# Kernel tuning notes

Hardware: AMD Instinct MI355X
Metric: run time of the kernel (lower is better)

The kernel has to match this reference:

```python
import jax, jax.numpy as jnp
import numpy as np

B, T, E, H, D = 2, 2048, 1024, 16, 64  # D = attention_dim // num_heads

def setup_inputs() -> dict:
    key = jax.random.key(0)
    k1, k2, k3, k4 = jax.random.split(key, 4)
    scale = 1.0 / np.sqrt(E)  # ~ torch Linear init scale
    embedded = jax.random.normal(k1, (B, T, E), dtype=jnp.float32)
    Wq = jax.random.normal(k2, (H, D, E), dtype=jnp.float32) * scale
    Wk = jax.random.normal(k3, (H, D, E), dtype=jnp.float32) * scale
    Wv = jax.random.normal(k4, (H, D, E), dtype=jnp.float32) * scale
    return {"embedded": embedded, "Wq": Wq, "Wk": Wk, "Wv": Wv}

def reference(embedded, Wq, Wk, Wv):
    # Batched multi-head projection (original loops per head; same math).
    q = jnp.einsum('bte,hde->bhtd', embedded, Wq)
    k = jnp.einsum('bte,hde->bhtd', embedded, Wk)
    v = jnp.einsum('bte,hde->bhtd', embedded, Wv)
    scores = jnp.einsum('bhtd,bhsd->bhts', q, k) / jnp.sqrt(jnp.float32(D))
    causal = jnp.tril(jnp.ones((T, T), dtype=bool))  # [T,T]
    scores = jnp.where(causal, scores, -jnp.inf)
    attn = jax.nn.softmax(scores, axis=-1)
    out = jnp.einsum('bhts,bhsd->bhtd', attn, v)
    # concat heads on last dim: [B,T,H*D]
    return out.transpose(0, 2, 1, 3).reshape(B, T, H * D)
```

## Files before the change

kernel.cpp:

```cpp
#include <hip/hip_runtime.h>
#include <hip/hip_bf16.h>
#include <stdint.h>

typedef __bf16 bf16_t;
typedef __bf16 bf16x8 __attribute__((ext_vector_type(8)));
typedef float  f32x4  __attribute__((ext_vector_type(4)));

#define LOG2E 1.44269504088896f

__device__ __forceinline__ void gload_lds16(const void* g, void* l) {
    __builtin_amdgcn_global_load_lds(
        (__attribute__((address_space(1))) unsigned int*)(uintptr_t)g,
        (__attribute__((address_space(3))) unsigned int*)(uint32_t)(uintptr_t)l,
        16, 0, 0);
}

__global__ __launch_bounds__(256) void convert_kernel(
    const float* __restrict__ emb, const float* __restrict__ wq,
    const float* __restrict__ wk,  const float* __restrict__ wv,
    bf16_t* __restrict__ embb, bf16_t* __restrict__ wcat)
{
    size_t base = ((size_t)blockIdx.x * 256 + threadIdx.x) * 8;
    const float* src;
    bf16_t* dst;
    if (base < (size_t)4194304) { src = emb + base; dst = embb + base; }
    else {
        size_t r = base - 4194304;
        int wsel = (int)(r >> 20);
        size_t off = r & 1048575;
        src = (wsel == 0 ? wq : (wsel == 1 ? wk : wv)) + off;
        dst = wcat + r;
    }
    float4 a  = *(const float4*)src;
    float4 c2 = *(const float4*)(src + 4);
    bf16x8 o;
    o[0]=(bf16_t)a.x;  o[1]=(bf16_t)a.y;  o[2]=(bf16_t)a.z;  o[3]=(bf16_t)a.w;
    o[4]=(bf16_t)c2.x; o[5]=(bf16_t)c2.y; o[6]=(bf16_t)c2.z; o[7]=(bf16_t)c2.w;
    *(bf16x8*)dst = o;
}

__global__ __launch_bounds__(256, 3) void proj_kernel(
    const bf16_t* __restrict__ A, const bf16_t* __restrict__ Wc,
    bf16_t* __restrict__ qo, bf16_t* __restrict__ ko, bf16_t* __restrict__ vto)
{
    __shared__ __align__(128) char smem[32768];

    const int tid  = threadIdx.x;
    const int w    = tid >> 6, lane = tid & 63;
    const int wr   = w >> 1,  wc2  = w & 1;
    const int g    = lane >> 4, c = lane & 15;
    const int bm   = blockIdx.x & 31, bn = blockIdx.x >> 5;
    const int m0   = bm * 128, n0 = bn * 128;

    f32x4 acc[4][4] = {};

    const int arow = lane >> 2;
    const int acol = (((lane & 3) ^ ((lane >> 3) & 3))) * 8;

    #define PROJ_STAGE(buf, kt)                                                        \
        do {                                                                           \
            char* As_ = smem + (buf) * 16384;                                          \
            char* Bs_ = As_ + 8192;                                                    \
            _Pragma("unroll")                                                          \
            for (int p = 0; p < 2; ++p) {                                              \
                gload_lds16(A  + (size_t)(m0 + p*64 + w*16 + arow) * 1024 + (kt)*32 + acol, \
                            As_ + (p*64 + w*16) * 64);                                 \
                gload_lds16(Wc + (size_t)(n0 + p*64 + w*16 + arow) * 1024 + (kt)*32 + acol, \
                            Bs_ + (p*64 + w*16) * 64);                                 \
            }                                                                          \
        } while (0)

    PROJ_STAGE(0, 0);
    __syncthreads();
    int cur = 0;
    for (int kt = 0; kt < 32; ++kt) {
        if (kt < 31) PROJ_STAGE(cur ^ 1, kt + 1);
        const char* As = smem + cur * 16384;
        const char* Bs = As + 8192;
        const int sw = (c >> 1) & 3;
        bf16x8 af[4], bf[4];
        #pragma unroll
        for (int i = 0; i < 4; ++i) {
            af[i] = *(const bf16x8*)(As + (wr*64  + i*16 + c) * 64 + ((g ^ sw) << 4));
            bf[i] = *(const bf16x8*)(Bs + (wc2*64 + i*16 + c) * 64 + ((g ^ sw) << 4));
        }
        #pragma unroll
        for (int i = 0; i < 4; ++i)
            #pragma unroll
            for (int j = 0; j < 4; ++j)
                acc[i][j] = __builtin_amdgcn_mfma_f32_16x16x32_bf16(af[i], bf[j], acc[i][j], 0, 0, 0);
        __syncthreads();
        cur ^= 1;
    }

    const int b  = m0 >> 11;
    const int t0 = m0 & 2047;

    if (n0 < 2048) {
        bf16_t* dst = (n0 < 1024) ? qo : ko;
        const int nl0 = n0 & 1023;
        #pragma unroll
        for (int i = 0; i < 4; ++i)
            #pragma unroll
            for (int j = 0; j < 4; ++j) {
                int dl = wc2*64 + j*16 + c;
                #pragma unroll
                for (int e = 0; e < 4; ++e) {
                    int tl = wr*64 + i*16 + g*4 + e;
                    *(bf16_t*)(smem + ((tl*256 + dl*2) ^ ((tl & 7) << 4))) = (bf16_t)acc[i][j][e];
                }
            }
        __syncthreads();
        #pragma unroll
        for (int it = 0; it < 8; ++it) {
            int chunk = it * 256 + tid;
            int tl = chunk >> 4;
            int ce = (chunk & 15) * 8;
            bf16x8 val = *(const bf16x8*)(smem + ((tl*256 + ce*2) ^ ((tl & 7) << 4)));
            int nn = nl0 + ce;
            int hh = nn >> 6, dd = nn & 63;
            *(bf16x8*)(dst + ((size_t)(b*16 + hh) * 2048 + (t0 + tl)) * 64 + dd) = val;
        }
    } else {
        #pragma unroll
        for (int i = 0; i < 4; ++i)
            #pragma unroll
            for (int j = 0; j < 4; ++j) {
                int dl = wc2*64 + j*16 + c;
                #pragma unroll
                for (int e = 0; e < 4; ++e) {
                    int tl = wr*64 + i*16 + g*4 + e;
                    *(bf16_t*)(smem + ((dl*256 + tl*2) ^ ((dl & 7) << 4))) = (bf16_t)acc[i][j][e];
                }
            }
        __syncthreads();
        const int nvbase = n0 - 2048;
        #pragma unroll
        for (int it = 0; it < 8; ++it) {
            int chunk = it * 256 + tid;
            int dl = chunk >> 4;
            int tc = (chunk & 15) * 8;
            bf16x8 val = *(const bf16x8*)(smem + ((dl*256 + tc*2) ^ ((dl & 7) << 4)));
            int nv = nvbase + dl;
            int hh = nv >> 6, dd = nv & 63;
            *(bf16x8*)(vto + (size_t)((b*16 + hh)*64 + dd) * 2048 + t0 + tc) = val;
        }
    }
    #undef PROJ_STAGE
}

__global__ __launch_bounds__(512, 4) void attn_kernel(
    const bf16_t* __restrict__ qg, const bf16_t* __restrict__ kg,
    const bf16_t* __restrict__ vtg, float* __restrict__ out)
{
    __shared__ __align__(128) char smem[49152];
    char* Ps = smem + 32768;

    const int tid = threadIdx.x;
    const int w = tid >> 6, lane = tid & 63;
    const int g = lane >> 4, c = lane & 15;
    const int id = blockIdx.x;
    const int qt = 15 - (id >> 5);
    const int bh = id & 31;
    const int b = bh >> 4, h = bh & 15;

    const bf16_t* qbase = qg  + (size_t)bh * 2048 * 64;
    const bf16_t* kbase = kg  + (size_t)bh * 2048 * 64;
    const bf16_t* vbase = vtg + (size_t)bh * 64 * 2048;
    float* obase = out + (size_t)b * 2048 * 1024 + h * 64;

    const int srow = lane >> 3;
    const int scol = ((lane & 7) ^ srow) * 8;

    const int q0 = qt * 128;
    const int nt = 2 * qt + 2;

    bf16x8 qf[2];
    #pragma unroll
    for (int kf = 0; kf < 2; ++kf) {
        bf16x8 v = *(const bf16x8*)(qbase + (size_t)(q0 + w*16 + c) * 64 + kf*32 + g*8);
        #pragma unroll
        for (int e = 0; e < 8; ++e) qf[kf][e] = (bf16_t)((float)v[e] * 0.125f);
    }

    f32x4 oacc[4] = {};
    float mrun[4], lrun[4];
    #pragma unroll
    for (int e = 0; e < 4; ++e) { mrun[e] = -INFINITY; lrun[e] = 0.0f; }

    #define ATTN_STAGE(buf, kt)                                                         \
        do {                                                                            \
            char* Kb_ = smem + (buf) * 16384;                                           \
            gload_lds16(kbase + (size_t)((kt)*64 + w*8 + srow) * 64 + scol, Kb_ + w*1024); \
            gload_lds16(vbase + (size_t)(w*8 + srow) * 2048 + (kt)*64 + scol,           \
                        Kb_ + 8192 + w*1024);                                           \
        } while (0)

    ATTN_STAGE(0, 0);
    __syncthreads();
    int cur = 0;

    for (int kt = 0; kt < nt; ++kt) {
        if (kt + 1 < nt) ATTN_STAGE(cur ^ 1, kt + 1);
        const char* Kb = smem + cur * 16384;
        const char* Vb = Kb + 8192;

        f32x4 sacc[4];
        #pragma unroll
        for (int ni = 0; ni < 4; ++ni) {
            int krow = ni*16 + c;
            bf16x8 k0 = *(const bf16x8*)(Kb + ((krow*128 +      g*16) ^ ((c & 7) << 4)));
            bf16x8 k1 = *(const bf16x8*)(Kb + ((krow*128 + 64 + g*16) ^ ((c & 7) << 4)));
            f32x4 s0 = {0.f, 0.f, 0.f, 0.f};
            s0 = __builtin_amdgcn_mfma_f32_16x16x32_bf16(qf[0], k0, s0, 0, 0, 0);
            s0 = __builtin_amdgcn_mfma_f32_16x16x32_bf16(qf[1], k1, s0, 0, 0, 0);
            sacc[ni] = s0;
        }

        if (kt >= 2*qt) {
            #pragma unroll
            for (int ni = 0; ni < 4; ++ni)
                #pragma unroll
                for (int e = 0; e < 4; ++e) {
                    int kk = kt*64 + ni*16 + c;
                    int qq = q0 + w*16 + g*4 + e;
                    if (kk > qq) sacc[ni][e] = -INFINITY;
                }
        }

        float sf[4];
        #pragma unroll
        for (int e = 0; e < 4; ++e) {
            float mx = fmaxf(fmaxf(sacc[0][e], sacc[1][e]),
                             fmaxf(sacc[2][e], sacc[3][e]));
            mx = fmaxf(mx, __shfl_xor(mx, 1));
            mx = fmaxf(mx, __shfl_xor(mx, 2));
            mx = fmaxf(mx, __shfl_xor(mx, 4));
            mx = fmaxf(mx, __shfl_xor(mx, 8));
            float mnew  = fmaxf(mrun[e], mx);
            float scale = exp2f((mrun[e] - mnew) * LOG2E);
            float ps = 0.f;
            #pragma unroll
            for (int ni = 0; ni < 4; ++ni) {
                float pv = exp2f((sacc[ni][e] - mnew) * LOG2E);
                sacc[ni][e] = pv;
                ps += pv;
            }
            ps += __shfl_xor(ps, 1);
            ps += __shfl_xor(ps, 2);
            ps += __shfl_xor(ps, 4);
            ps += __shfl_xor(ps, 8);
            lrun[e] = lrun[e] * scale + ps;
            mrun[e] = mnew;
            sf[e]   = scale;
        }
        #pragma unroll
        for (int db = 0; db < 4; ++db)
            #pragma unroll
            for (int e = 0; e < 4; ++e)
                oacc[db][e] *= sf[e];

        #pragma unroll
        for (int ni = 0; ni < 4; ++ni)
            #pragma unroll
            for (int e = 0; e < 4; ++e) {
                int row = w*16 + g*4 + e;
                *(bf16_t*)(Ps + ((row*128 + (ni*16 + c)*2) ^ ((row & 7) << 4))) =
                    (bf16_t)sacc[ni][e];
            }

        bf16x8 pfr[2];
        {
            int prow = w*16 + c;
            pfr[0] = *(const bf16x8*)(Ps + ((prow*128 +      g*16) ^ ((prow & 7) << 4)));
            pfr[1] = *(const bf16x8*)(Ps + ((prow*128 + 64 + g*16) ^ ((prow & 7) << 4)));
        }
        #pragma unroll
        for (int db = 0; db < 4; ++db) {
            int vrow = db*16 + c;
            bf16x8 v0 = *(const bf16x8*)(Vb + ((vrow*128 +      g*16) ^ ((c & 7) << 4)));
            bf16x8 v1 = *(const bf16x8*)(Vb + ((vrow*128 + 64 + g*16) ^ ((c & 7) << 4)));
            oacc[db] = __builtin_amdgcn_mfma_f32_16x16x32_bf16(pfr[0], v0, oacc[db], 0, 0, 0);
            oacc[db] = __builtin_amdgcn_mfma_f32_16x16x32_bf16(pfr[1], v1, oacc[db], 0, 0, 0);
        }

        __syncthreads();
        cur ^= 1;
    }

    #pragma unroll
    for (int e = 0; e < 4; ++e) {
        float inv = 1.0f / lrun[e];
        size_t trow = (size_t)(q0 + w*16 + g*4 + e);
        #pragma unroll
        for (int db = 0; db < 4; ++db)
            obase[trow * 1024 + db*16 + c] = oacc[db][e] * inv;
    }
    #undef ATTN_STAGE
}

extern "C" void kernel_launch(void* const* d_in, const int* in_sizes, int n_in,
                              void* d_out, int out_size, void* d_ws, size_t ws_size,
                              hipStream_t stream) {
    const float* emb = (const float*)d_in[0];
    const float* wq  = (const float*)d_in[1];
    const float* wk  = (const float*)d_in[2];
    const float* wv  = (const float*)d_in[3];
    float* out = (float*)d_out;

    char* ws = (char*)d_ws;
    bf16_t* embb = (bf16_t*)ws;
    bf16_t* wcat = (bf16_t*)(ws + (size_t) 8*1024*1024);
    bf16_t* qb   = (bf16_t*)(ws + (size_t)14*1024*1024);
    bf16_t* kb   = (bf16_t*)(ws + (size_t)22*1024*1024);
    bf16_t* vtb  = (bf16_t*)(ws + (size_t)30*1024*1024);

    convert_kernel<<<3584, 256, 0, stream>>>(emb, wq, wk, wv, embb, wcat);
    proj_kernel<<<768, 256, 0, stream>>>(embb, wcat, qb, kb, vtb);
    attn_kernel<<<512, 512, 0, stream>>>(qb, kb, vtb, out);
}
```

Measured before the change: 180.8 us.

## Triple-buffer proj and attention loads, keep P in registers, lazy softmax rescale

The projection GEMM moves from a double buffer to a three-stage LDS ring with explicit vmcnt waits and raw barriers, so loads run two tiles ahead. The attention kernel shrinks to 64-query blocks of 256 threads over twice as many blocks, with the same three-stage ring. It computes S transposed so each lane holds one query row, builds P in registers without an LDS round trip, and folds log2e into the Q scale. It also rescales the output only when the running max grows by more than 8. This cuts barriers, LDS traffic and exp work, but adds more blocks and a more fragile wait-count scheme.

```diff
diff --git a/kernel.cpp b/kernel.cpp
--- a/kernel.cpp
+++ b/kernel.cpp
@@ -3,10 +3,11 @@
 #include <stdint.h>
 
 typedef __bf16 bf16_t;
+typedef __bf16 bf16x4 __attribute__((ext_vector_type(4)));
 typedef __bf16 bf16x8 __attribute__((ext_vector_type(8)));
 typedef float  f32x4  __attribute__((ext_vector_type(4)));
 
-#define LOG2E 1.44269504088896f
+#define QK_SCALE 0.1803368801111204f
 
 __device__ __forceinline__ void gload_lds16(const void* g, void* l) {
     __builtin_amdgcn_global_load_lds(
@@ -43,7 +44,7 @@
     const bf16_t* __restrict__ A, const bf16_t* __restrict__ Wc,
     bf16_t* __restrict__ qo, bf16_t* __restrict__ ko, bf16_t* __restrict__ vto)
 {
-    __shared__ __align__(128) char smem[32768];
+    __shared__ __align__(128) char smem[49152];
 
     const int tid  = threadIdx.x;
     const int w    = tid >> 6, lane = tid & 63;
@@ -71,10 +72,17 @@
         } while (0)
 
     PROJ_STAGE(0, 0);
-    __syncthreads();
+    PROJ_STAGE(1, 1);
     int cur = 0;
     for (int kt = 0; kt < 32; ++kt) {
-        if (kt < 31) PROJ_STAGE(cur ^ 1, kt + 1);
+        if (kt == 31) asm volatile("s_waitcnt vmcnt(0)" ::: "memory");
+        else          asm volatile("s_waitcnt vmcnt(4)" ::: "memory");
+        __builtin_amdgcn_s_barrier();
+        asm volatile("" ::: "memory");
+        if (kt + 2 < 32) {
+            int b2 = cur + 2; if (b2 >= 3) b2 -= 3;
+            PROJ_STAGE(b2, kt + 2);
+        }
         const char* As = smem + cur * 16384;
         const char* Bs = As + 8192;
         const int sw = (c >> 1) & 3;
@@ -89,9 +97,9 @@
             #pragma unroll
             for (int j = 0; j < 4; ++j)
                 acc[i][j] = __builtin_amdgcn_mfma_f32_16x16x32_bf16(af[i], bf[j], acc[i][j], 0, 0, 0);
-        __syncthreads();
-        cur ^= 1;
-    }
+        cur = (cur == 2) ? 0 : cur + 1;
+    }
+    __syncthreads();
 
     const int b  = m0 >> 11;
     const int t0 = m0 & 2047;
@@ -149,18 +157,17 @@
     #undef PROJ_STAGE
 }
 
-__global__ __launch_bounds__(512, 4) void attn_kernel(
+__global__ __launch_bounds__(256, 3) void attn_kernel(
     const bf16_t* __restrict__ qg, const bf16_t* __restrict__ kg,
     const bf16_t* __restrict__ vtg, float* __restrict__ out)
 {
     __shared__ __align__(128) char smem[49152];
-    char* Ps = smem + 32768;
 
     const int tid = threadIdx.x;
     const int w = tid >> 6, lane = tid & 63;
     const int g = lane >> 4, c = lane & 15;
     const int id = blockIdx.x;
-    const int qt = 15 - (id >> 5);
+    const int qt = 31 - (id >> 5);
     const int bh = id & 31;
     const int b = bh >> 4, h = bh & 15;
 
@@ -172,129 +179,136 @@
     const int srow = lane >> 3;
     const int scol = ((lane & 7) ^ srow) * 8;
 
-    const int q0 = qt * 128;
-    const int nt = 2 * qt + 2;
+    const int q0 = qt * 64;
+    const int nt = qt + 1;
 
     bf16x8 qf[2];
     #pragma unroll
     for (int kf = 0; kf < 2; ++kf) {
         bf16x8 v = *(const bf16x8*)(qbase + (size_t)(q0 + w*16 + c) * 64 + kf*32 + g*8);
         #pragma unroll
-        for (int e = 0; e < 8; ++e) qf[kf][e] = (bf16_t)((float)v[e] * 0.125f);
+        for (int e = 0; e < 8; ++e) qf[kf][e] = (bf16_t)((float)v[e] * QK_SCALE);
     }
 
     f32x4 oacc[4] = {};
-    float mrun[4], lrun[4];
-    #pragma unroll
-    for (int e = 0; e < 4; ++e) { mrun[e] = -INFINITY; lrun[e] = 0.0f; }
-
-    #define ATTN_STAGE(buf, kt)                                                         \
-        do {                                                                            \
-            char* Kb_ = smem + (buf) * 16384;                                           \
-            gload_lds16(kbase + (size_t)((kt)*64 + w*8 + srow) * 64 + scol, Kb_ + w*1024); \
-            gload_lds16(vbase + (size_t)(w*8 + srow) * 2048 + (kt)*64 + scol,           \
-                        Kb_ + 8192 + w*1024);                                           \
+    float mrun = -INFINITY, lrun = 0.0f;
+
+    #define ATTN_STAGE(buf, kt)                                                          \
+        do {                                                                             \
+            char* Kb_ = smem + (buf) * 16384;                                            \
+            _Pragma("unroll")                                                            \
+            for (int j = 0; j < 2; ++j) {                                                \
+                gload_lds16(kbase + (size_t)((kt)*64 + w*16 + j*8 + srow) * 64 + scol,   \
+                            Kb_ + (w*16 + j*8) * 128);                                   \
+                gload_lds16(vbase + (size_t)(w*16 + j*8 + srow) * 2048 + (kt)*64 + scol, \
+                            Kb_ + 8192 + (w*16 + j*8) * 128);                            \
+            }                                                                            \
         } while (0)
 
     ATTN_STAGE(0, 0);
-    __syncthreads();
+    if (nt > 1) ATTN_STAGE(1, 1);
     int cur = 0;
 
     for (int kt = 0; kt < nt; ++kt) {
-        if (kt + 1 < nt) ATTN_STAGE(cur ^ 1, kt + 1);
-        const char* Kb = smem + cur * 16384;
-        const char* Vb = Kb + 8192;
+        if (kt == nt - 1) asm volatile("s_waitcnt vmcnt(0)" ::: "memory");
+        else              asm volatile("s_waitcnt vmcnt(4)" ::: "memory");
+        __builtin_amdgcn_s_barrier();
+        asm volatile("" ::: "memory");
+        if (kt + 2 < nt) {
+            int b2 = cur + 2; if (b2 >= 3) b2 -= 3;
+            ATTN_STAGE(b2, kt + 2);
+        }
+        const char* Ks = smem + cur * 16384;
+        const char* Vs = Ks + 8192;
 
         f32x4 sacc[4];
         #pragma unroll
         for (int ni = 0; ni < 4; ++ni) {
             int krow = ni*16 + c;
-            bf16x8 k0 = *(const bf16x8*)(Kb + ((krow*128 +      g*16) ^ ((c & 7) << 4)));
-            bf16x8 k1 = *(const bf16x8*)(Kb + ((krow*128 + 64 + g*16) ^ ((c & 7) << 4)));
+            bf16x8 k0 = *(const bf16x8*)(Ks + krow*128 + ((     g*16) ^ ((c & 7) << 4)));
+            bf16x8 k1 = *(const bf16x8*)(Ks + krow*128 + ((64 + g*16) ^ ((c & 7) << 4)));
             f32x4 s0 = {0.f, 0.f, 0.f, 0.f};
-            s0 = __builtin_amdgcn_mfma_f32_16x16x32_bf16(qf[0], k0, s0, 0, 0, 0);
-            s0 = __builtin_amdgcn_mfma_f32_16x16x32_bf16(qf[1], k1, s0, 0, 0, 0);
+            s0 = __builtin_amdgcn_mfma_f32_16x16x32_bf16(k0, qf[0], s0, 0, 0, 0);
+            s0 = __builtin_amdgcn_mfma_f32_16x16x32_bf16(k1, qf[1], s0, 0, 0, 0);
             sacc[ni] = s0;
         }
 
-        if (kt >= 2*qt) {
+        if (kt == nt - 1) {
+            const int qloc = w*16 + c;
             #pragma unroll
             for (int ni = 0; ni < 4; ++ni)
                 #pragma unroll
-                for (int e = 0; e < 4; ++e) {
-                    int kk = kt*64 + ni*16 + c;
-                    int qq = q0 + w*16 + g*4 + e;
-                    if (kk > qq) sacc[ni][e] = -INFINITY;
-                }
-        }
-
-        float sf[4];
-        #pragma unroll
-        for (int e = 0; e < 4; ++e) {
-            float mx = fmaxf(fmaxf(sacc[0][e], sacc[1][e]),
-                             fmaxf(sacc[2][e], sacc[3][e]));
-            mx = fmaxf(mx, __shfl_xor(mx, 1));
-            mx = fmaxf(mx, __shfl_xor(mx, 2));
-            mx = fmaxf(mx, __shfl_xor(mx, 4));
-            mx = fmaxf(mx, __shfl_xor(mx, 8));
-            float mnew  = fmaxf(mrun[e], mx);
-            float scale = exp2f((mrun[e] - mnew) * LOG2E);
-            float ps = 0.f;
-            #pragma unroll
-            for (int ni = 0; ni < 4; ++ni) {
-                float pv = exp2f((sacc[ni][e] - mnew) * LOG2E);
-                sacc[ni][e] = pv;
-                ps += pv;
+                for (int e = 0; e < 4; ++e)
+                    if (ni*16 + g*4 + e > qloc) sacc[ni][e] = -INFINITY;
+        }
+
+        float pmax;
+        {
+            float a0 = fmaxf(fmaxf(sacc[0][0], sacc[0][1]), fmaxf(sacc[0][2], sacc[0][3]));
+            float a1 = fmaxf(fmaxf(sacc[1][0], sacc[1][1]), fmaxf(sacc[1][2], sacc[1][3]));
+            float a2 = fmaxf(fmaxf(sacc[2][0], sacc[2][1]), fmaxf(sacc[2][2], sacc[2][3]));
+            float a3 = fmaxf(fmaxf(sacc[3][0], sacc[3][1]), fmaxf(sacc[3][2], sacc[3][3]));
+            pmax = fmaxf(fmaxf(a0, a1), fmaxf(a2, a3));
+            pmax = fmaxf(pmax, __shfl_xor(pmax, 16));
+            pmax = fmaxf(pmax, __shfl_xor(pmax, 32));
+        }
+
+        if (__any(pmax > mrun + 8.0f)) {
+            float mnew = fmaxf(mrun, pmax);
+            float sc = exp2f(mrun - mnew);
+            float s0_ = __shfl(sc, g*4 + 0);
+            float s1_ = __shfl(sc, g*4 + 1);
+            float s2_ = __shfl(sc, g*4 + 2);
+            float s3_ = __shfl(sc, g*4 + 3);
+            #pragma unroll
+            for (int db = 0; db < 4; ++db) {
+                oacc[db][0] *= s0_; oacc[db][1] *= s1_;
+                oacc[db][2] *= s2_; oacc[db][3] *= s3_;
             }
-            ps += __shfl_xor(ps, 1);
-            ps += __shfl_xor(ps, 2);
-            ps += __shfl_xor(ps, 4);
-            ps += __shfl_xor(ps, 8);
-            lrun[e] = lrun[e] * scale + ps;
-            mrun[e] = mnew;
-            sf[e]   = scale;
-        }
-        #pragma unroll
-        for (int db = 0; db < 4; ++db)
-            #pragma unroll
-            for (int e = 0; e < 4; ++e)
-                oacc[db][e] *= sf[e];
-
+            lrun *= sc;
+            mrun = mnew;
+        }
+
+        float psum = 0.f;
+        bf16x8 palo, pahi;
         #pragma unroll
         for (int ni = 0; ni < 4; ++ni)
             #pragma unroll
             for (int e = 0; e < 4; ++e) {
-                int row = w*16 + g*4 + e;
-                *(bf16_t*)(Ps + ((row*128 + (ni*16 + c)*2) ^ ((row & 7) << 4))) =
-                    (bf16_t)sacc[ni][e];
+                float pv = exp2f(sacc[ni][e] - mrun);
+                psum += pv;
+                if (ni < 2) palo[(ni & 1)*4 + e] = (bf16_t)pv;
+                else        pahi[(ni & 1)*4 + e] = (bf16_t)pv;
             }
-
-        bf16x8 pfr[2];
-        {
-            int prow = w*16 + c;
-            pfr[0] = *(const bf16x8*)(Ps + ((prow*128 +      g*16) ^ ((prow & 7) << 4)));
-            pfr[1] = *(const bf16x8*)(Ps + ((prow*128 + 64 + g*16) ^ ((prow & 7) << 4)));
-        }
+        psum += __shfl_xor(psum, 16);
+        psum += __shfl_xor(psum, 32);
+        lrun += psum;
+
         #pragma unroll
         for (int db = 0; db < 4; ++db) {
             int vrow = db*16 + c;
-            bf16x8 v0 = *(const bf16x8*)(Vb + ((vrow*128 +      g*16) ^ ((c & 7) << 4)));
-            bf16x8 v1 = *(const bf16x8*)(Vb + ((vrow*128 + 64 + g*16) ^ ((c & 7) << 4)));
-            oacc[db] = __builtin_amdgcn_mfma_f32_16x16x32_bf16(pfr[0], v0, oacc[db], 0, 0, 0);
-            oacc[db] = __builtin_amdgcn_mfma_f32_16x16x32_bf16(pfr[1], v1, oacc[db], 0, 0, 0);
-        }
-
-        __syncthreads();
-        cur ^= 1;
-    }
-
+            bf16x4 v0 = *(const bf16x4*)(Vs + vrow*128 + ((     g*8) ^ ((c & 7) << 4)));
+            bf16x4 v1 = *(const bf16x4*)(Vs + vrow*128 + ((32 + g*8) ^ ((c & 7) << 4)));
+            bf16x4 v2 = *(const bf16x4*)(Vs + vrow*128 + ((64 + g*8) ^ ((c & 7) << 4)));
+            bf16x4 v3 = *(const bf16x4*)(Vs + vrow*128 + ((96 + g*8) ^ ((c & 7) << 4)));
+            bf16x8 vlo = __builtin_shufflevector(v0, v1, 0, 1, 2, 3, 4, 5, 6, 7);
+            bf16x8 vhi = __builtin_shufflevector(v2, v3, 0, 1, 2, 3, 4, 5, 6, 7);
+            oacc[db] = __builtin_amdgcn_mfma_f32_16x16x32_bf16(palo, vlo, oacc[db], 0, 0, 0);
+            oacc[db] = __builtin_amdgcn_mfma_f32_16x16x32_bf16(pahi, vhi, oacc[db], 0, 0, 0);
+        }
+
+        cur = (cur == 2) ? 0 : cur + 1;
+    }
+
+    float inv[4];
+    #pragma unroll
+    for (int e = 0; e < 4; ++e) inv[e] = 1.0f / __shfl(lrun, g*4 + e);
     #pragma unroll
     for (int e = 0; e < 4; ++e) {
-        float inv = 1.0f / lrun[e];
         size_t trow = (size_t)(q0 + w*16 + g*4 + e);
         #pragma unroll
         for (int db = 0; db < 4; ++db)
-            obase[trow * 1024 + db*16 + c] = oacc[db][e] * inv;
+            obase[trow * 1024 + db*16 + c] = oacc[db][e] * inv[e];
     }
     #undef ATTN_STAGE
 }
@@ -317,5 +331,5 @@
 
     convert_kernel<<<3584, 256, 0, stream>>>(emb, wq, wk, wv, embb, wcat);
     proj_kernel<<<768, 256, 0, stream>>>(embb, wcat, qb, kb, vtb);
-    attn_kernel<<<512, 512, 0, stream>>>(qb, kb, vtb, out);
-}
+    attn_kernel<<<1024, 256, 0, stream>>>(qb, kb, vtb, out);
+}
```

Measured after the change: 154.4 us. 14.6% less time.
